# Optimization experiments

Hardware: AMD Instinct MI355X
Metric: run time of the kernel (lower is better)

## Reference

```python
import jax, jax.numpy as jnp
import numpy as np

LOSS_WEIGHT = 1.0
BIG = 1e9  # finite sentinel for masked-out pixels (avoids inf-grad NaNs)


def setup_inputs() -> dict:
    key = jax.random.key(0)
    k1, k2 = jax.random.split(key)
    B, N, H, W = 4, 6890, 64, 64
    vert2d = jax.random.uniform(k1, (B, N, 2), dtype=jnp.float32) * jnp.array([W, H], jnp.float32)
    mask = jax.random.randint(k2, (B, H, W), 0, 2, dtype=jnp.int32)
    return {"vert2d": vert2d, "mask": mask}


def reference(vert2d, mask):
    B, N, _ = vert2d.shape
    _, H, W = mask.shape
    scale = jnp.array([W, H], vert2d.dtype)
    v = vert2d / scale  # [B,N,2], normalized
    # all pixel coords as (x, y), normalized -- the dense equivalent of torch.where points
    ys, xs = jnp.meshgrid(jnp.arange(H), jnp.arange(W), indexing="ij")
    pts = (jnp.stack([xs.ravel(), ys.ravel()], axis=-1).astype(v.dtype) / scale)  # [HW,2]
    valid = (mask.reshape(B, -1) > 0)  # [B,HW] boolean membership of each pixel
    # pairwise L2 distances: [B,N,HW]
    diff = v[:, :, None, :] - pts[None, None, :, :]
    d = jnp.sqrt(jnp.sum(diff * diff, axis=-1))
    dm = jnp.where(valid[:, None, :], d, BIG)
    # sum over mask points of min over verts  +  sum over verts of min over mask points
    loss = jnp.sum(jnp.min(dm, axis=1) * valid) + jnp.sum(jnp.min(dm, axis=2))
    return LOSS_WEIGHT * loss
```

## Files before the change

### kernel.cpp

```cpp
#include <hip/hip_runtime.h>

#define NB 4
#define NV 6890
#define HW 4096
#define NPAD 6912
#define T1CS 216
#define T1_BLOCKS 256
#define T2_BLOCKS 256
#define NELEM 44032
#define NRED_BLOCKS 16

#define OFF_T1  0
#define OFF_T2  65536

#define FINF 3.402823466e38f
#define PBIG 1.0e18f

__global__ __launch_bounds__(256) void k_main(const float* __restrict__ vert,
                                              const int* __restrict__ mask,
                                              unsigned* __restrict__ t1,
                                              unsigned* __restrict__ t2) {
    __shared__ float4 lds4[T1CS];
    float2* lds2 = reinterpret_cast<float2*>(lds4);
    int bx = blockIdx.x, tid = threadIdx.x;
    if (bx < T1_BLOCKS) {
        int c = bx & 31, q = (bx >> 5) & 1, b = bx >> 6;
        if (tid < T1CS) {
            int n = c * T1CS + tid;
            float4 w = make_float4(0.f, 0.f, PBIG, 0.f);
            if (n < NV) {
                float2 v = reinterpret_cast<const float2*>(vert)[b * NV + n];
                w = make_float4(-2.f * v.x, -2.f * v.y, fmaf(v.x, v.x, v.y * v.y), 0.f);
            }
            lds4[tid] = w;
        }
        __syncthreads();
        int x = tid & 63, ry = tid >> 6;
        float fx = (float)x;
        float fy[8], m[8];
        #pragma unroll
        for (int k = 0; k < 8; ++k) { fy[k] = (float)(q * 32 + ry + 4 * k); m[k] = FINF; }
        #pragma unroll 4
        for (int i = 0; i < T1CS; i += 2) {
            float4 a = lds4[i], g2 = lds4[i + 1];
            float ta = fmaf(a.x,  fx, a.z);
            float tg = fmaf(g2.x, fx, g2.z);
            #pragma unroll
            for (int k = 0; k < 8; ++k)
                m[k] = fminf(m[k], fminf(fmaf(a.y, fy[k], ta), fmaf(g2.y, fy[k], tg)));
        }
        float fx2 = fx * fx;
        unsigned* tp = t1 + (b << 12) + x;
        #pragma unroll
        for (int k = 0; k < 8; ++k) {
            int y = q * 32 + ry + 4 * k;
            float mf = fmaxf(fmaf(fy[k], fy[k], fx2) + m[k], 0.f);
            atomicMin(tp + y * 64, __float_as_uint(mf));
        }
    } else {
        int t2i = bx - T1_BLOCKS;
        int pc = t2i & 31, g = (t2i >> 5) & 1, b = t2i >> 6;
        if (tid < 128) {
            int r = tid >> 6, j = tid & 63;
            int pix = (pc * 2 + r) * 64 + j;
            float fx = (float)j;
            float e = (mask[b * HW + pix] > 0) ? fx * fx : PBIG;
            lds2[tid] = make_float2(-2.f * fx, e);
        }
        __syncthreads();
        int n0 = g * 4096 + tid;
        const float2* vv2 = reinterpret_cast<const float2*>(vert) + b * NV;
        float vx[16], vy[16], vv[16], acc[16];
        bool val[16];
        #pragma unroll
        for (int k = 0; k < 16; ++k) {
            int n = n0 + 256 * k;
            val[k] = (n < NV);
            float2 t = val[k] ? vv2[n] : make_float2(0.f, 0.f);
            vx[k] = t.x; vy[k] = t.y;
            vv[k] = fmaf(t.x, t.x, t.y * t.y);
        }
        #pragma unroll
        for (int r = 0; r < 2; ++r) {
            float fyr  = (float)(pc * 2 + r);
            float fm2y = -2.f * fyr;
            float mr[16];
            #pragma unroll
            for (int k = 0; k < 16; ++k) mr[k] = FINF;
            #pragma unroll 2
            for (int j = 0; j < 64; j += 2) {
                float2 a = lds2[r * 64 + j], cc = lds2[r * 64 + j + 1];
                #pragma unroll
                for (int k = 0; k < 16; ++k) {
                    float da = fmaf(a.x,  vx[k], a.y);
                    float dc = fmaf(cc.x, vx[k], cc.y);
                    mr[k] = fminf(mr[k], fminf(da, dc));
                }
            }
            #pragma unroll
            for (int k = 0; k < 16; ++k) {
                float base = fmaf(fm2y, vy[k], fmaf(fyr, fyr, vv[k]));
                float rv = mr[k] + base;
                acc[k] = r ? fminf(acc[k], rv) : rv;
            }
        }
        unsigned* op = t2 + b * NPAD + n0;
        #pragma unroll
        for (int k = 0; k < 16; ++k)
            if (val[k]) {
                float mf = fmaxf(acc[k], 0.f);
                atomicMin(op + 256 * k, __float_as_uint(mf));
            }
    }
}

__global__ __launch_bounds__(256) void k_red(const unsigned* __restrict__ t1,
                                             const unsigned* __restrict__ t2,
                                             const int* __restrict__ mask,
                                             float* __restrict__ out) {
    int tid = threadIdx.x;
    float v = 0.f;
    for (int gid = blockIdx.x * 256 + tid; gid < NELEM; gid += NRED_BLOCKS * 256) {
        float e = 0.f;
        if (gid < NB * HW) {
            if (mask[gid] > 0)
                e = sqrtf(fmaxf(__uint_as_float(t1[gid]), 0.f));
        } else {
            int j = gid - NB * HW;
            int b = j / NPAD;
            int n = j - b * NPAD;
            if (n < NV)
                e = sqrtf(fmaxf(__uint_as_float(t2[j]), 0.f));
        }
        v += e;
    }
    v *= (1.0f / 64.0f);
    __shared__ float sbuf[4];
    for (int off = 32; off; off >>= 1) v += __shfl_down(v, off, 64);
    int lane = tid & 63, wid = tid >> 6;
    if (!lane) sbuf[wid] = v;
    __syncthreads();
    if (tid == 0)
        atomicAdd(out, sbuf[0] + sbuf[1] + sbuf[2] + sbuf[3]);
}

extern "C" void kernel_launch(void* const* d_in, const int* in_sizes, int n_in,
                              void* d_out, int out_size, void* d_ws, size_t ws_size,
                              hipStream_t stream) {
    const float* vert = (const float*)d_in[0];
    const int*   mask = (const int*)d_in[1];
    char* ws = (char*)d_ws;
    unsigned* t1  = (unsigned*)(ws + OFF_T1);
    unsigned* t2  = (unsigned*)(ws + OFF_T2);
    float*    out = (float*)d_out;

    k_main<<<T1_BLOCKS + T2_BLOCKS, 256, 0, stream>>>(vert, mask, t1, t2);
    k_red <<<NRED_BLOCKS, 256, 0, stream>>>(t1, t2, mask, out);
}
```

Baseline: 75.09 us.

## Double block count with smaller vertex chunks and per-row pixel tiles

Splits the work into twice as many blocks: the vertex-to-pixel pass loads 108 raw vertices per block and computes the -2v terms and squared norms inside the loop, and the pixel-to-vertex pass handles one mask row per block. LDS reads become float4 to fetch two entries at once, and the per-row accumulation into a running min is removed. The aim is more parallelism and shorter per-block loops to improve occupancy and latency hiding on the large GPU. In exchange there are more atomicMin operations, extra ALU work per vertex pair in the first pass, and each vertex load is repeated across twice as many blocks.

```diff
diff --git a/kernel.cpp b/kernel.cpp
--- a/kernel.cpp
+++ b/kernel.cpp
@@ -4,9 +4,9 @@
 #define NV 6890
 #define HW 4096
 #define NPAD 6912
-#define T1CS 216
-#define T1_BLOCKS 256
-#define T2_BLOCKS 256
+#define T1CS 108
+#define T1_BLOCKS 512
+#define T2_BLOCKS 512
 #define NELEM 44032
 #define NRED_BLOCKS 16
 
@@ -14,101 +14,97 @@
 #define OFF_T2  65536
 
 #define FINF 3.402823466e38f
+#define VBIG 1.0e9f
 #define PBIG 1.0e18f
 
 __global__ __launch_bounds__(256) void k_main(const float* __restrict__ vert,
                                               const int* __restrict__ mask,
                                               unsigned* __restrict__ t1,
                                               unsigned* __restrict__ t2) {
-    __shared__ float4 lds4[T1CS];
+    __shared__ float4 lds4[64];
     float2* lds2 = reinterpret_cast<float2*>(lds4);
     int bx = blockIdx.x, tid = threadIdx.x;
     if (bx < T1_BLOCKS) {
-        int c = bx & 31, q = (bx >> 5) & 1, b = bx >> 6;
+        int c = bx & 63, q = (bx >> 6) & 1, b = bx >> 7;
         if (tid < T1CS) {
             int n = c * T1CS + tid;
-            float4 w = make_float4(0.f, 0.f, PBIG, 0.f);
-            if (n < NV) {
-                float2 v = reinterpret_cast<const float2*>(vert)[b * NV + n];
-                w = make_float4(-2.f * v.x, -2.f * v.y, fmaf(v.x, v.x, v.y * v.y), 0.f);
-            }
-            lds4[tid] = w;
+            float2 w = make_float2(VBIG, 0.f);
+            if (n < NV) w = reinterpret_cast<const float2*>(vert)[b * NV + n];
+            lds2[tid] = w;
         }
         __syncthreads();
         int x = tid & 63, ry = tid >> 6;
         float fx = (float)x;
-        float fy[8], m[8];
+        float fm2x = -2.f * fx, fx2 = fx * fx;
+        float fm2y[8], m[8];
         #pragma unroll
-        for (int k = 0; k < 8; ++k) { fy[k] = (float)(q * 32 + ry + 4 * k); m[k] = FINF; }
-        #pragma unroll 4
-        for (int i = 0; i < T1CS; i += 2) {
-            float4 a = lds4[i], g2 = lds4[i + 1];
-            float ta = fmaf(a.x,  fx, a.z);
-            float tg = fmaf(g2.x, fx, g2.z);
+        for (int k = 0; k < 8; ++k) {
+            fm2y[k] = -2.f * (float)(q * 32 + ry + 4 * k);
+            m[k] = FINF;
+        }
+        #pragma unroll 6
+        for (int i = 0; i < T1CS / 2; ++i) {
+            float4 a = lds4[i];
+            float vva = fmaf(a.x, a.x, a.y * a.y);
+            float vvb = fmaf(a.z, a.z, a.w * a.w);
+            float ta  = fmaf(fm2x, a.x, vva);
+            float tb  = fmaf(fm2x, a.z, vvb);
             #pragma unroll
-            for (int k = 0; k < 8; ++k)
-                m[k] = fminf(m[k], fminf(fmaf(a.y, fy[k], ta), fmaf(g2.y, fy[k], tg)));
+            for (int k = 0; k < 8; ++k) {
+                float da = fmaf(fm2y[k], a.y, ta);
+                float db = fmaf(fm2y[k], a.w, tb);
+                m[k] = fminf(m[k], fminf(da, db));
+            }
         }
-        float fx2 = fx * fx;
         unsigned* tp = t1 + (b << 12) + x;
         #pragma unroll
         for (int k = 0; k < 8; ++k) {
             int y = q * 32 + ry + 4 * k;
-            float mf = fmaxf(fmaf(fy[k], fy[k], fx2) + m[k], 0.f);
+            float fy = (float)y;
+            float mf = fmaxf(fmaf(fy, fy, fx2) + m[k], 0.f);
             atomicMin(tp + y * 64, __float_as_uint(mf));
         }
     } else {
         int t2i = bx - T1_BLOCKS;
-        int pc = t2i & 31, g = (t2i >> 5) & 1, b = t2i >> 6;
-        if (tid < 128) {
-            int r = tid >> 6, j = tid & 63;
-            int pix = (pc * 2 + r) * 64 + j;
-            float fx = (float)j;
+        int y = t2i & 63, rest = t2i >> 6;
+        int g = rest & 1, b = rest >> 1;
+        if (tid < 64) {
+            int pix = y * 64 + tid;
+            float fx = (float)tid;
             float e = (mask[b * HW + pix] > 0) ? fx * fx : PBIG;
             lds2[tid] = make_float2(-2.f * fx, e);
         }
         __syncthreads();
         int n0 = g * 4096 + tid;
         const float2* vv2 = reinterpret_cast<const float2*>(vert) + b * NV;
-        float vx[16], vy[16], vv[16], acc[16];
+        float fy = (float)y, fm2y = -2.f * fy;
+        float vx[16], base[16], mr[16];
         bool val[16];
         #pragma unroll
         for (int k = 0; k < 16; ++k) {
             int n = n0 + 256 * k;
             val[k] = (n < NV);
             float2 t = val[k] ? vv2[n] : make_float2(0.f, 0.f);
-            vx[k] = t.x; vy[k] = t.y;
-            vv[k] = fmaf(t.x, t.x, t.y * t.y);
+            vx[k] = t.x;
+            float vv = fmaf(t.x, t.x, t.y * t.y);
+            base[k] = fmaf(fm2y, t.y, fmaf(fy, fy, vv));
+            mr[k] = FINF;
         }
-        #pragma unroll
-        for (int r = 0; r < 2; ++r) {
-            float fyr  = (float)(pc * 2 + r);
-            float fm2y = -2.f * fyr;
-            float mr[16];
-            #pragma unroll
-            for (int k = 0; k < 16; ++k) mr[k] = FINF;
-            #pragma unroll 2
-            for (int j = 0; j < 64; j += 2) {
-                float2 a = lds2[r * 64 + j], cc = lds2[r * 64 + j + 1];
-                #pragma unroll
-                for (int k = 0; k < 16; ++k) {
-                    float da = fmaf(a.x,  vx[k], a.y);
-                    float dc = fmaf(cc.x, vx[k], cc.y);
-                    mr[k] = fminf(mr[k], fminf(da, dc));
-                }
-            }
+        #pragma unroll 4
+        for (int j = 0; j < 32; ++j) {
+            float4 a = lds4[j];
             #pragma unroll
             for (int k = 0; k < 16; ++k) {
-                float base = fmaf(fm2y, vy[k], fmaf(fyr, fyr, vv[k]));
-                float rv = mr[k] + base;
-                acc[k] = r ? fminf(acc[k], rv) : rv;
+                float da = fmaf(a.x, vx[k], a.y);
+                float db = fmaf(a.z, vx[k], a.w);
+                mr[k] = fminf(mr[k], fminf(da, db));
             }
         }
         unsigned* op = t2 + b * NPAD + n0;
         #pragma unroll
         for (int k = 0; k < 16; ++k)
             if (val[k]) {
-                float mf = fmaxf(acc[k], 0.f);
+                float mf = fmaxf(mr[k] + base[k], 0.f);
                 atomicMin(op + 256 * k, __float_as_uint(mf));
             }
     }
```

Result: no change. 74.30 us (median of 2 runs) (-1.0%).
